# Kernel tuning notes

Hardware: AMD Instinct MI355X
Metric: run time of the kernel (lower is better)

## Reference

```python
import jax, jax.numpy as jnp
import numpy as np
import math

B, NOUT, NCLASSES, CENTER, TOPK = 1024, 512, 5994, 3, 5
M, SUB_M, SCALE = 0.2, -0.06, 30.0

COS_M, SIN_M = math.cos(M), math.sin(M)
TH, MM = math.cos(math.pi - M), math.sin(math.pi - M) * M
SUB_COS_M, SUB_SIN_M = math.cos(SUB_M), math.sin(SUB_M)
SUB_TH, SUB_MM = math.cos(math.pi - SUB_M), math.sin(math.pi - SUB_M) * SUB_M


def setup_inputs() -> dict:
    key = jax.random.key(0)
    k1, k2, k3 = jax.random.split(key, 3)
    x = jax.random.normal(k1, (B, NOUT), dtype=jnp.float32)
    # xavier_normal over (center, nClasses, nOut): fan_in=nClasses*nOut, fan_out=center*nOut
    std = math.sqrt(2.0 / (NCLASSES * NOUT + CENTER * NOUT))
    weight = jax.random.normal(k2, (CENTER, NCLASSES, NOUT), dtype=jnp.float32) * std
    label = jax.random.randint(k3, (B,), 0, NCLASSES, dtype=jnp.int64)
    return {"x": x, "weight": weight, "label": label}


def _l2norm(v, axis=-1, eps=1e-12):
    return v / jnp.maximum(jnp.linalg.norm(v, axis=axis, keepdims=True), eps)


def reference(x, weight, label):
    xn = _l2norm(x)                       # [B, j]
    wn = _l2norm(weight)                  # [a, c, j]
    cosine_subcen = jnp.einsum('bj,acj->bac', xn, wn)   # [B, center, C]
    cosine = jnp.max(cosine_subcen, axis=1)             # [B, C]

    sine = jnp.sqrt(jnp.clip(1.0 - cosine * cosine, 0.0, 1.0))
    phi = jnp.where(cosine - TH > 0, cosine * COS_M - sine * SIN_M, cosine - MM)
    sub_phi = jnp.where(cosine - SUB_TH > 0,
                        cosine * SUB_COS_M - sine * SUB_SIN_M,
                        cosine - SUB_MM)

    # topk+1 candidates; drop the label column if present, else drop the last
    _, idx = jax.lax.top_k(cosine, TOPK + 1)            # [B, topk+1]
    is_label = (idx == label[:, None].astype(idx.dtype))
    # stable sort pushes the (unique) label hit to the end, preserving order otherwise
    order = jnp.argsort(is_label.astype(jnp.int32), axis=1, stable=True)
    idx_fixed = jnp.take_along_axis(idx, order[:, :TOPK], axis=1)   # [B, topk]

    rows = jnp.arange(B)[:, None]
    one_hot_sub = jnp.zeros_like(cosine).at[rows, idx_fixed].add(1.0)
    one_hot = jax.nn.one_hot(label, NCLASSES, dtype=cosine.dtype)

    output = (one_hot * phi + one_hot_sub * sub_phi
              + (1.0 - one_hot_sub - one_hot) * cosine) * SCALE

    logp = jax.nn.log_softmax(output, axis=-1)
    loss = -jnp.mean(logp[jnp.arange(B), label])

    pred = jnp.argmax(cosine * SCALE, axis=-1)
    prec1 = jnp.mean((pred == label).astype(jnp.float32)) * 100.0
    return loss, prec1
```

## Files before the change

### kernel.cpp

```cpp
#include <hip/hip_runtime.h>
#include <math.h>

#define NB 1024
#define NC 5994
#define NCP 6144
#define NCS 6016
#define NK 512
#define NA 3
#define NT 48
#define SCALE_F 30.0f

#define COS_M_F 0.9800665778412416f
#define SIN_M_F 0.19866933079506122f
#define TH_F (-0.9800665778412416f)
#define MM_F 0.039733866159012244f
#define SUB_COS_M_F 0.9982005399352042f
#define SUB_SIN_M_F (-0.05996400647944459f)
#define SUB_TH_F (-0.9982005399352042f)
#define SUB_MM_F 0.0035978403887666754f

typedef __attribute__((ext_vector_type(8))) short short8;
typedef __attribute__((ext_vector_type(8))) unsigned short ushort8;
typedef __attribute__((ext_vector_type(4))) float f32x4;

__device__ __forceinline__ float waveReduceSum(float v) {
#pragma unroll
  for (int off = 32; off > 0; off >>= 1) v += __shfl_down(v, off);
  return v;
}

__device__ __forceinline__ void waveArgMax(float& v, int& i) {
#pragma unroll
  for (int off = 32; off > 0; off >>= 1) {
    float ov = __shfl_down(v, off);
    int oi = __shfl_down(i, off);
    if (ov > v || (ov == v && (unsigned)oi < (unsigned)i)) { v = ov; i = oi; }
  }
}

__device__ __forceinline__ ushort f2bf(float f) {
  unsigned u = __float_as_uint(f);
  u += 0x7FFFu + ((u >> 16) & 1u);
  return (ushort)(u >> 16);
}

__device__ __forceinline__ float bf2f(ushort u) {
  return __uint_as_float(((unsigned)u) << 16);
}

__device__ __forceinline__ void load_lds16(const ushort* g, ushort* l) {
  __builtin_amdgcn_global_load_lds(
      (const __attribute__((address_space(1))) unsigned int*)g,
      (__attribute__((address_space(3))) unsigned int*)l, 16, 0, 0);
}

__global__ __launch_bounds__(256) void norm_convert(const float* __restrict__ x,
                                                    const float* __restrict__ w,
                                                    ushort* __restrict__ xb,
                                                    ushort* __restrict__ wb) {
  const int row = blockIdx.x * 4 + (threadIdx.x >> 6);
  const int lane = threadIdx.x & 63;
  const float* src;
  ushort* dst;
  if (row < NB) {
    src = x + (size_t)row * NK;
    dst = xb + (size_t)row * NK;
  } else {
    const int r = row - NB;
    const int a = r / NCP, c = r % NCP;
    dst = wb + (size_t)r * NK;
    if (c >= NC) {
      ushort4 z = {0, 0, 0, 0};
      *(ushort4*)(dst + lane * 4) = z;
      *(ushort4*)(dst + 256 + lane * 4) = z;
      return;
    }
    src = w + ((size_t)a * NC + c) * NK;
  }
  const float4 v0 = *(const float4*)(src + lane * 4);
  const float4 v1 = *(const float4*)(src + 256 + lane * 4);
  float ss = v0.x * v0.x + v0.y * v0.y + v0.z * v0.z + v0.w * v0.w +
             v1.x * v1.x + v1.y * v1.y + v1.z * v1.z + v1.w * v1.w;
  ss = waveReduceSum(ss);
  ss = __shfl(ss, 0);
  const float rn = 1.0f / fmaxf(sqrtf(ss), 1e-12f);
  ushort4 o0 = {f2bf(v0.x * rn), f2bf(v0.y * rn), f2bf(v0.z * rn), f2bf(v0.w * rn)};
  ushort4 o1 = {f2bf(v1.x * rn), f2bf(v1.y * rn), f2bf(v1.z * rn), f2bf(v1.w * rn)};
  *(ushort4*)(dst + lane * 4) = o0;
  *(ushort4*)(dst + 256 + lane * 4) = o1;
}

__global__ __launch_bounds__(64) void cos_gemm_mfma(const ushort* __restrict__ Xb,
                                                    const ushort* __restrict__ Wb,
                                                    ushort* __restrict__ cosb) {
  __shared__ ushort sA0[2048], sA1[2048];
  __shared__ ushort sB0[2048], sB1[2048];
  const int lane = threadIdx.x;

  const int id = blockIdx.x;
  const int cx = (id & 7) + ((id >> 7) << 3);
  const int by = (id >> 3) & 15;
  const int b0 = by * 64;
  const int c0 = cx * 64;

  const int lrow = lane >> 2;
  const int skg = ((lane & 3) - ((lane >> 3) & 3)) & 3;
  const ushort* gA = Xb + (size_t)(b0 + lrow) * NK + skg * 8;
  const ushort* gB = Wb + (size_t)(c0 + lrow) * NK + skg * 8;

  const int r = lane & 15;
  const int kg = lane >> 4;
  const int rdoff = r * 32 + (((kg + (r >> 1)) & 3) * 8);

  f32x4 best[4][4];
  f32x4 acc[4][4];
#pragma unroll
  for (int i = 0; i < 4; ++i)
#pragma unroll
    for (int j = 0; j < 4; ++j) {
#pragma unroll
      for (int q = 0; q < 4; ++q) best[i][j][q] = -INFINITY;
      acc[i][j] = (f32x4)(0.f);
    }

#define STAGE(TT, SAw, SBw)                                                     \
  {                                                                             \
    const int tt_ = (TT);                                                       \
    const int k0 = (tt_ & 15) << 5;                                             \
    const size_t boff = (size_t)(tt_ >> 4) * NCP * NK + k0;                     \
    _Pragma("unroll") for (int s = 0; s < 4; ++s) {                             \
      load_lds16(gA + (size_t)s * 16 * NK + k0, (ushort*)SAw + s * 512);        \
      load_lds16(gB + (size_t)s * 16 * NK + boff, (ushort*)SBw + s * 512);      \
    }                                                                           \
  }

  STAGE(0, sA0, sB0)
  __syncthreads();

#define GEMM_BODY(T, SAr, SBr, SAw, SBw)                                        \
  {                                                                             \
    const int t_ = (T);                                                         \
    if (t_ + 1 < NT) STAGE(t_ + 1, SAw, SBw)                                    \
    short8 af[4], bf[4];                                                        \
    _Pragma("unroll") for (int mi = 0; mi < 4; ++mi)                            \
        af[mi] = *(const short8*)&SAr[mi * 512 + rdoff];                        \
    _Pragma("unroll") for (int ni = 0; ni < 4; ++ni)                            \
        bf[ni] = *(const short8*)&SBr[ni * 512 + rdoff];                        \
    _Pragma("unroll") for (int mi = 0; mi < 4; ++mi)                            \
        _Pragma("unroll") for (int ni = 0; ni < 4; ++ni)                        \
            acc[mi][ni] = __builtin_amdgcn_mfma_f32_16x16x32_bf16(              \
                af[mi], bf[ni], acc[mi][ni], 0, 0, 0);                          \
    if ((t_ & 15) == 15) {                                                      \
      _Pragma("unroll") for (int i = 0; i < 4; ++i)                             \
          _Pragma("unroll") for (int j = 0; j < 4; ++j) {                       \
        _Pragma("unroll") for (int q = 0; q < 4; ++q)                           \
            best[i][j][q] = fmaxf(best[i][j][q], acc[i][j][q]);                 \
        acc[i][j] = (f32x4)(0.f);                                               \
      }                                                                         \
    }                                                                           \
    __syncthreads();                                                            \
  }

  for (int t = 0; t < NT; t += 2) {
    GEMM_BODY(t, sA0, sB0, sA1, sB1)
    GEMM_BODY(t + 1, sA1, sB1, sA0, sB0)
  }
#undef GEMM_BODY
#undef STAGE

  const int q4 = (lane >> 4) * 4;
#pragma unroll
  for (int ni = 0; ni < 4; ++ni) {
    const int col = c0 + ni * 16 + r;
    if (col < NC) {
#pragma unroll
      for (int mi = 0; mi < 4; ++mi) {
        const int row0 = b0 + mi * 16 + q4;
#pragma unroll
        for (int q = 0; q < 4; ++q)
          cosb[(size_t)(row0 + q) * NCS + col] = f2bf(best[mi][ni][q]);
      }
    }
  }
}

__global__ __launch_bounds__(256) void row_loss(const ushort* __restrict__ cosb,
                                                const int* __restrict__ label,
                                                float* __restrict__ loss_b,
                                                float* __restrict__ corr_b) {
  __shared__ float swv[4];
  __shared__ int swi[4];
  __shared__ float s_red[4];
  __shared__ float s_maxv;
  __shared__ float s_cosL;
  __shared__ float topv[6];
  __shared__ int topi[6];

  const int b = blockIdx.x, tid = threadIdx.x;
  const int wv = tid >> 6;
  const int lab = label[b];
  const ushort* row = cosb + (size_t)b * NCS;

  float v[24];
  float bv = -INFINITY;
  int bi = -1;
#pragma unroll
  for (int j = 0; j < 3; ++j) {
    const ushort8 u = *(const ushort8*)(row + j * 2048 + tid * 8);
#pragma unroll
    for (int e = 0; e < 8; ++e) {
      const int idx = j * 2048 + tid * 8 + e;
      const float f = (idx < NC) ? bf2f(u[e]) : -INFINITY;
      v[j * 8 + e] = f;
      if (f > bv) { bv = f; bi = idx; }
      if (idx == lab) s_cosL = f;
    }
  }
  waveArgMax(bv, bi);
  if ((tid & 63) == 0) { swv[wv] = bv; swi[wv] = bi; }
  __syncthreads();
  if (tid == 0) {
    float mv = swv[0]; int mi = swi[0];
    for (int q = 1; q < 4; ++q)
      if (swv[q] > mv || (swv[q] == mv && (unsigned)swi[q] < (unsigned)mi)) { mv = swv[q]; mi = swi[q]; }
    s_maxv = mv; topv[0] = mv; topi[0] = mi;
  }
  __syncthreads();
  const float maxv = s_maxv;

  float ps = 0.f;
#pragma unroll
  for (int j = 0; j < 24; ++j) ps += __expf(SCALE_F * (v[j] - maxv));
  ps = waveReduceSum(ps);
  if ((tid & 63) == 0) s_red[wv] = ps;

  unsigned excl = 0;
  {
    const int wi = topi[0];
    if (((wi & 2047) >> 3) == tid) excl |= 1u << (((wi >> 11) << 3) | (wi & 7));
  }

  for (int e = 1; e < 6; ++e) {
    float lv = -INFINITY;
    int li = -1;
#pragma unroll
    for (int j = 0; j < 3; ++j)
#pragma unroll
      for (int k = 0; k < 8; ++k) {
        const int s = j * 8 + k;
        if (!((excl >> s) & 1u) && v[s] > lv) { lv = v[s]; li = j * 2048 + tid * 8 + k; }
      }
    waveArgMax(lv, li);
    if ((tid & 63) == 0) { swv[wv] = lv; swi[wv] = li; }
    __syncthreads();
    if (tid == 0) {
      float mv = swv[0]; int mi = swi[0];
      for (int q = 1; q < 4; ++q)
        if (swv[q] > mv || (swv[q] == mv && (unsigned)swi[q] < (unsigned)mi)) { mv = swv[q]; mi = swi[q]; }
      topv[e] = mv; topi[e] = mi;
    }
    __syncthreads();
    const int wi = topi[e];
    if (((wi & 2047) >> 3) == tid) excl |= 1u << (((wi >> 11) << 3) | (wi & 7));
  }

  if (tid == 0) {
    const float S = s_red[0] + s_red[1] + s_red[2] + s_red[3];
    const float m = SCALE_F * maxv;
    const float cosL = s_cosL;
    const float sineL = sqrtf(fminf(fmaxf(1.f - cosL * cosL, 0.f), 1.f));
    const float phiL = (cosL - TH_F > 0.f) ? (cosL * COS_M_F - sineL * SIN_M_F) : (cosL - MM_F);
    float adj = __expf(SCALE_F * phiL - m) - __expf(SCALE_F * cosL - m);
    int cnt = 0;
    for (int e = 0; e < 6 && cnt < 5; ++e) {
      if (topi[e] == lab) continue;
      const float c = topv[e];
      const float sine = sqrtf(fminf(fmaxf(1.f - c * c, 0.f), 1.f));
      const float sp = (c - SUB_TH_F > 0.f) ? (c * SUB_COS_M_F - sine * SUB_SIN_M_F) : (c - SUB_MM_F);
      adj += __expf(SCALE_F * sp - m) - __expf(SCALE_F * c - m);
      ++cnt;
    }
    const float Sp = S + adj;
    loss_b[b] = (logf(Sp) + m) - SCALE_F * phiL;
    corr_b[b] = (topi[0] == lab) ? 1.f : 0.f;
  }
}

__global__ __launch_bounds__(256) void finalize(const float* __restrict__ loss_b,
                                                const float* __restrict__ corr_b,
                                                float* __restrict__ out) {
  const int tid = threadIdx.x;
  float ls = 0.f, cs = 0.f;
  for (int i = tid; i < NB; i += 256) { ls += loss_b[i]; cs += corr_b[i]; }
  ls = waveReduceSum(ls);
  cs = waveReduceSum(cs);
  __shared__ float sl[4], sc[4];
  if ((tid & 63) == 0) { sl[tid >> 6] = ls; sc[tid >> 6] = cs; }
  __syncthreads();
  if (tid == 0) {
    const float L = sl[0] + sl[1] + sl[2] + sl[3];
    const float Cr = sc[0] + sc[1] + sc[2] + sc[3];
    out[0] = L / (float)NB;
    out[1] = Cr / (float)NB * 100.f;
  }
}

extern "C" void kernel_launch(void* const* d_in, const int* in_sizes, int n_in,
                              void* d_out, int out_size, void* d_ws, size_t ws_size,
                              hipStream_t stream) {
  const float* x = (const float*)d_in[0];
  const float* w = (const float*)d_in[1];
  const int* label = (const int*)d_in[2];
  float* out = (float*)d_out;
  char* ws = (char*)d_ws;

  ushort* xb = (ushort*)ws;
  ushort* wb = (ushort*)(ws + 1048576);
  ushort* cosb = (ushort*)(ws + 1048576 + 18874368);
  float* loss_b = (float*)ws;
  float* corr_b = (float*)(ws + 4096);

  norm_convert<<<(NB + NA * NCP) / 4, 256, 0, stream>>>(x, w, xb, wb);
  cos_gemm_mfma<<<16 * 96, 64, 0, stream>>>(xb, wb, cosb);
  row_loss<<<NB, 256, 0, stream>>>(cosb, label, loss_b, corr_b);
  finalize<<<1, 256, 0, stream>>>(loss_b, corr_b, out);
}
```

Baseline: 66.92 us.

## Load MFMA operands directly from global into registers, dropping LDS staging

The GEMM kernel no longer stages A/B tiles through double-buffered shared memory with global_load_lds and barriers. Each lane now loads its MFMA fragments straight from global memory into registers, using register double buffering with a fully unrolled loop. This removes the LDS round trip and the per-step __syncthreads. The cost is that each 16-byte fragment is fetched by only one lane in a 64-thread block with no reuse across lanes, so the kernel leans on L1/L2 and adds register pressure from the unroll.

```diff
diff --git a/kernel.cpp b/kernel.cpp
--- a/kernel.cpp
+++ b/kernel.cpp
@@ -46,12 +46,6 @@
 
 __device__ __forceinline__ float bf2f(ushort u) {
   return __uint_as_float(((unsigned)u) << 16);
-}
-
-__device__ __forceinline__ void load_lds16(const ushort* g, ushort* l) {
-  __builtin_amdgcn_global_load_lds(
-      (const __attribute__((address_space(1))) unsigned int*)g,
-      (__attribute__((address_space(3))) unsigned int*)l, 16, 0, 0);
 }
 
 __global__ __launch_bounds__(256) void norm_convert(const float* __restrict__ x,
@@ -93,8 +87,6 @@
 __global__ __launch_bounds__(64) void cos_gemm_mfma(const ushort* __restrict__ Xb,
                                                     const ushort* __restrict__ Wb,
                                                     ushort* __restrict__ cosb) {
-  __shared__ ushort sA0[2048], sA1[2048];
-  __shared__ ushort sB0[2048], sB1[2048];
   const int lane = threadIdx.x;
 
   const int id = blockIdx.x;
@@ -103,14 +95,10 @@
   const int b0 = by * 64;
   const int c0 = cx * 64;
 
-  const int lrow = lane >> 2;
-  const int skg = ((lane & 3) - ((lane >> 3) & 3)) & 3;
-  const ushort* gA = Xb + (size_t)(b0 + lrow) * NK + skg * 8;
-  const ushort* gB = Wb + (size_t)(c0 + lrow) * NK + skg * 8;
-
   const int r = lane & 15;
   const int kg = lane >> 4;
-  const int rdoff = r * 32 + (((kg + (r >> 1)) & 3) * 8);
+  const ushort* pA = Xb + (size_t)(b0 + r) * NK + kg * 8;
+  const ushort* pB = Wb + (size_t)(c0 + r) * NK + kg * 8;
 
   f32x4 best[4][4];
   f32x4 acc[4][4];
@@ -123,34 +111,26 @@
       acc[i][j] = (f32x4)(0.f);
     }
 
-#define STAGE(TT, SAw, SBw)                                                     \
+  short8 af0[4], bf0[4], af1[4], bf1[4];
+
+#define LOADF(TT, AF, BF)                                                       \
   {                                                                             \
     const int tt_ = (TT);                                                       \
     const int k0 = (tt_ & 15) << 5;                                             \
     const size_t boff = (size_t)(tt_ >> 4) * NCP * NK + k0;                     \
-    _Pragma("unroll") for (int s = 0; s < 4; ++s) {                             \
-      load_lds16(gA + (size_t)s * 16 * NK + k0, (ushort*)SAw + s * 512);        \
-      load_lds16(gB + (size_t)s * 16 * NK + boff, (ushort*)SBw + s * 512);      \
-    }                                                                           \
-  }
-
-  STAGE(0, sA0, sB0)
-  __syncthreads();
-
-#define GEMM_BODY(T, SAr, SBr, SAw, SBw)                                        \
+    _Pragma("unroll") for (int mi = 0; mi < 4; ++mi)                            \
+        AF[mi] = *(const short8*)(pA + (size_t)mi * 16 * NK + k0);              \
+    _Pragma("unroll") for (int ni = 0; ni < 4; ++ni)                            \
+        BF[ni] = *(const short8*)(pB + (size_t)ni * 16 * NK + boff);            \
+  }
+
+#define MFMA16(AF, BF, T)                                                       \
   {                                                                             \
-    const int t_ = (T);                                                         \
-    if (t_ + 1 < NT) STAGE(t_ + 1, SAw, SBw)                                    \
-    short8 af[4], bf[4];                                                        \
-    _Pragma("unroll") for (int mi = 0; mi < 4; ++mi)                            \
-        af[mi] = *(const short8*)&SAr[mi * 512 + rdoff];                        \
-    _Pragma("unroll") for (int ni = 0; ni < 4; ++ni)                            \
-        bf[ni] = *(const short8*)&SBr[ni * 512 + rdoff];                        \
     _Pragma("unroll") for (int mi = 0; mi < 4; ++mi)                            \
         _Pragma("unroll") for (int ni = 0; ni < 4; ++ni)                        \
             acc[mi][ni] = __builtin_amdgcn_mfma_f32_16x16x32_bf16(              \
-                af[mi], bf[ni], acc[mi][ni], 0, 0, 0);                          \
-    if ((t_ & 15) == 15) {                                                      \
+                AF[mi], BF[ni], acc[mi][ni], 0, 0, 0);                          \
+    if (((T) & 15) == 15) {                                                     \
       _Pragma("unroll") for (int i = 0; i < 4; ++i)                             \
           _Pragma("unroll") for (int j = 0; j < 4; ++j) {                       \
         _Pragma("unroll") for (int q = 0; q < 4; ++q)                           \
@@ -158,17 +138,20 @@
         acc[i][j] = (f32x4)(0.f);                                               \
       }                                                                         \
     }                                                                           \
-    __syncthreads();                                                            \
-  }
-
+  }
+
+  LOADF(0, af0, bf0)
+#pragma unroll
   for (int t = 0; t < NT; t += 2) {
-    GEMM_BODY(t, sA0, sB0, sA1, sB1)
-    GEMM_BODY(t + 1, sA1, sB1, sA0, sB0)
-  }
-#undef GEMM_BODY
-#undef STAGE
-
-  const int q4 = (lane >> 4) * 4;
+    if (t + 1 < NT) LOADF(t + 1, af1, bf1)
+    MFMA16(af0, bf0, t)
+    if (t + 2 < NT) LOADF(t + 2, af0, bf0)
+    MFMA16(af1, bf1, t + 1)
+  }
+#undef LOADF
+#undef MFMA16
+
+  const int q4 = kg * 4;
 #pragma unroll
   for (int ni = 0; ni < 4; ++ni) {
     const int col = c0 + ni * 16 + r;
```

Result: slower. 98.30 us (+46.9%).
